# Performance work log

Measured on AMD Instinct MI355X. Metric: run time of the kernel, lower is better.

The kernel has to match this reference:

```python
import jax, jax.numpy as jnp
import numpy as np

B, C, H, W, T_PREV, HEADS, KSIZE = 16, 512, 28, 28, 15, 16, 5


def setup_inputs() -> dict:
    key = jax.random.key(0)
    ks = jax.random.split(key, 6)
    return {
        "x": jax.random.normal(ks[0], (B, C, H, W), jnp.float32),
        "prev_K": jax.random.normal(ks[1], (B, T_PREV, C), jnp.float32),
        "prev_V": jax.random.normal(ks[2], (B, T_PREV, C, H, W), jnp.float32) * 0.1,
        "wq": jax.random.normal(ks[3], (1, 1, KSIZE), jnp.float32) * 0.3,
        "wk": jax.random.normal(ks[4], (1, 1, KSIZE), jnp.float32) * 0.3,
        "wv": jax.random.normal(ks[5], (C, 1, 3, 3), jnp.float32) * 0.2,
    }


def _conv1d_same(y, ker):
    # y: [b,1,c], ker: [1,1,k]; SAME padding = (k-1)//2 on each side for odd k
    p = (ker.shape[-1] - 1) // 2
    return jax.lax.conv_general_dilated(
        y, ker, (1,), [(p, p)], dimension_numbers=("NCH", "OIH", "NCH"))


def _forward(x, prev_K, prev_V, wq, wk, wv):
    b, c, h, w = x.shape
    g = HEADS
    d = c // g
    norm = 1.0 / jnp.sqrt(jnp.asarray(d, x.dtype))
    # ECA-style channel attention: global avg pool -> conv1d over channels
    y = jnp.mean(x, axis=(2, 3))[:, None, :]            # [b,1,c]
    Q = _conv1d_same(y, wq)[:, 0, :]                    # [b,c]
    k = _conv1d_same(y, wk)                             # [b,1,c]
    # depthwise 3x3 conv for V
    v = jax.lax.conv_general_dilated(
        x, wv, (1, 1), [(1, 1), (1, 1)],
        dimension_numbers=("NCHW", "OIHW", "NCHW"), feature_group_count=c)
    # grow recurrent caches
    K = jnp.concatenate([prev_K, k], axis=1)            # [b,t,c]
    V = jnp.concatenate([prev_V, v[:, None]], axis=1)   # [b,t,c,h,w]
    t = K.shape[1]
    # grouped decode attention: single query step vs t cached steps
    Qg = Q.reshape(b, g, d)                             # [b,g,d]
    Kg = K.reshape(b, t, g, d)                          # [b,t,g,d]
    atten = jnp.einsum("bgd,btgd->bgt", Qg, Kg) * norm  # [b,g,t]
    atten = jax.nn.softmax(atten, axis=-1)
    Vg = V.reshape(b, t, g, d, h, w)                    # [b,t,g,d,h,w]
    out = jnp.einsum("bgt,btgdhw->bgdhw", atten, Vg).reshape(b, c, h, w)
    return out, K, V


def reference(x, prev_K, prev_V, wq, wk, wv):
    return _forward(x, prev_K, prev_V, wq, wk, wv)
```

## Files before the change

### kernel.cpp

```cpp
#include <hip/hip_runtime.h>
#include <hip/hip_bf16.h>

#define B_ 16
#define C_ 512
#define H_ 28
#define W_ 28
#define TPREV 15
#define TT 16
#define HEADS_ 16
#define DHEAD 32
#define HW 784
#define HW4 196
#define CH4 (C_ * HW4)
#define NORM 0.17677669529663687f

typedef float f32x4 __attribute__((ext_vector_type(4)));

__global__ __launch_bounds__(64) void pool_kernel(const float* __restrict__ x,
                                                  float* __restrict__ y) {
    const int bc = blockIdx.x;
    const f32x4* __restrict__ xr = (const f32x4*)(x + (size_t)bc * HW);
    const int lane = threadIdx.x;
    float s = 0.0f;
    for (int i = lane; i < HW4; i += 64) {
        f32x4 v = xr[i];
        s += v.x + v.y + v.z + v.w;
    }
    #pragma unroll
    for (int off = 32; off > 0; off >>= 1) s += __shfl_down(s, off);
    if (lane == 0) y[bc] = s * (1.0f / (float)HW);
}

__global__ __launch_bounds__(256) void attn_kernel(const float* __restrict__ y,
                                                   const float* __restrict__ prevK,
                                                   const float* __restrict__ wq,
                                                   const float* __restrict__ wk,
                                                   float* __restrict__ Kout,
                                                   float* __restrict__ att) {
    const int b = blockIdx.x;
    const int tid = threadIdx.x;
    __shared__ float y_s[C_];
    __shared__ float Q_s[C_];
    __shared__ float K_s[TT * 513];
    __shared__ float logit[HEADS_][17];

    y_s[tid]       = y[b * C_ + tid];
    y_s[tid + 256] = y[b * C_ + tid + 256];

    const float q0 = wq[0], q1 = wq[1], q2 = wq[2], q3 = wq[3], q4 = wq[4];
    const float k0 = wk[0], k1 = wk[1], k2 = wk[2], k3 = wk[3], k4 = wk[4];

    for (int i = tid; i < TPREV * C_; i += 256) {
        int t = i >> 9, c = i & (C_ - 1);
        K_s[t * 513 + c] = prevK[((size_t)b * TPREV + t) * C_ + c];
    }
    __syncthreads();

    for (int c = tid; c < C_; c += 256) {
        float a0 = (c >= 2)      ? y_s[c - 2] : 0.0f;
        float a1 = (c >= 1)      ? y_s[c - 1] : 0.0f;
        float a2 = y_s[c];
        float a3 = (c <= C_ - 2) ? y_s[c + 1] : 0.0f;
        float a4 = (c <= C_ - 3) ? y_s[c + 2] : 0.0f;
        Q_s[c]               = a0 * q0 + a1 * q1 + a2 * q2 + a3 * q3 + a4 * q4;
        K_s[TPREV * 513 + c] = a0 * k0 + a1 * k1 + a2 * k2 + a3 * k3 + a4 * k4;
    }
    __syncthreads();

    for (int i = tid; i < TT * C_; i += 256) {
        int t = i >> 9, c = i & (C_ - 1);
        Kout[((size_t)b * TT + t) * C_ + c] = K_s[t * 513 + c];
    }

    const int g = tid >> 4, t = tid & 15;
    float s = 0.0f;
    #pragma unroll
    for (int d = 0; d < DHEAD; ++d)
        s += Q_s[g * DHEAD + d] * K_s[t * 513 + g * DHEAD + d];
    s *= NORM;
    logit[g][t] = s;
    __syncthreads();

    float m = -1e30f;
    #pragma unroll
    for (int j = 0; j < TT; ++j) m = fmaxf(m, logit[g][j]);
    float sum = 0.0f;
    #pragma unroll
    for (int j = 0; j < TT; ++j) sum += __expf(logit[g][j] - m);
    att[((size_t)b * HEADS_ + g) * TT + t] = __expf(s - m) / sum;
}

__global__ __launch_bounds__(256) void fuse_kernel(const float* __restrict__ x,
                                                   const float* __restrict__ prevV,
                                                   const float* __restrict__ wv,
                                                   const float* __restrict__ att,
                                                   float* __restrict__ out,
                                                   float* __restrict__ Vout) {
    const int i = blockIdx.x * 256 + threadIdx.x;
    const int p4 = i % HW4;
    const int bc = i / HW4;
    const int c  = bc & (C_ - 1);
    const int b  = bc >> 9;
    const int g  = c >> 5;

    const float* __restrict__ xbc = x + (size_t)bc * HW;
    const int p  = p4 * 4;
    const int h  = p / W_;
    const int w0 = p % W_;
    float r[3][6];
    #pragma unroll
    for (int ry = 0; ry < 3; ++ry) {
        const int hh = h - 1 + ry;
        if (hh < 0 || hh >= H_) {
            #pragma unroll
            for (int j = 0; j < 6; ++j) r[ry][j] = 0.0f;
        } else {
            const float* row = xbc + hh * W_;
            f32x4 mid = *(const f32x4*)(row + w0);
            r[ry][1] = mid.x; r[ry][2] = mid.y; r[ry][3] = mid.z; r[ry][4] = mid.w;
            r[ry][0] = (w0 > 0)      ? row[w0 - 1] : 0.0f;
            r[ry][5] = (w0 + 4 < W_) ? row[w0 + 4] : 0.0f;
        }
    }
    float wv9[9];
    #pragma unroll
    for (int k = 0; k < 9; ++k) wv9[k] = wv[c * 9 + k];

    f32x4 v4;
    #pragma unroll
    for (int j = 0; j < 4; ++j) {
        float s = 0.0f;
        #pragma unroll
        for (int ky = 0; ky < 3; ++ky)
            #pragma unroll
            for (int kx = 0; kx < 3; ++kx)
                s = fmaf(r[ky][j + kx], wv9[ky * 3 + kx], s);
        v4[j] = s;
    }

    const float* __restrict__ arow = att + ((size_t)b * HEADS_ + g) * TT;

    f32x4* __restrict__ Vo = (f32x4*)Vout;
    const f32x4* __restrict__ Pv = (const f32x4*)prevV;
    const size_t pvq = ((size_t)b * TPREV * C_ + c) * HW4 + p4;
    const size_t voq = ((size_t)b * TT    * C_ + c) * HW4 + p4;

    f32x4 pv[TPREV];
    #pragma unroll
    for (int t = 0; t < TPREV; ++t)
        pv[t] = __builtin_nontemporal_load(&Pv[pvq + (size_t)t * CH4]);

    f32x4 acc;
    {
        const float a = arow[TPREV];
        __builtin_nontemporal_store(v4, &Vo[voq + (size_t)TPREV * CH4]);
        acc = v4 * a;
    }

    #pragma unroll
    for (int t = 0; t < TPREV; ++t) {
        __builtin_nontemporal_store(pv[t], &Vo[voq + (size_t)t * CH4]);
        const float a = arow[t];
        acc.x = fmaf(a, pv[t].x, acc.x);
        acc.y = fmaf(a, pv[t].y, acc.y);
        acc.z = fmaf(a, pv[t].z, acc.z);
        acc.w = fmaf(a, pv[t].w, acc.w);
    }
    __builtin_nontemporal_store(acc, &((f32x4*)out)[(size_t)bc * HW4 + p4]);
}

extern "C" void kernel_launch(void* const* d_in, const int* in_sizes, int n_in,
                              void* d_out, int out_size, void* d_ws, size_t ws_size,
                              hipStream_t stream) {
    const float* x     = (const float*)d_in[0];
    const float* prevK = (const float*)d_in[1];
    const float* prevV = (const float*)d_in[2];
    const float* wq    = (const float*)d_in[3];
    const float* wk    = (const float*)d_in[4];
    const float* wv    = (const float*)d_in[5];

    float* out  = (float*)d_out;
    float* Kout = out + (size_t)B_ * C_ * HW;
    float* Vout = Kout + (size_t)B_ * TT * C_;

    float* y_ws   = (float*)d_ws;
    float* att_ws = y_ws + B_ * C_;

    pool_kernel<<<B_ * C_, 64, 0, stream>>>(x, y_ws);
    attn_kernel<<<B_, 256, 0, stream>>>(y_ws, prevK, wq, wk, Kout, att_ws);

    const int totalq = B_ * C_ * HW4;
    fuse_kernel<<<totalq / 256, 256, 0, stream>>>(x, prevV, wv, att_ws, out, Vout);
}
```

Baseline: 161.0 us.

## Fold attention computation into fuse kernel and merge K copy into pool kernel

Removes the separate 16-block attention kernel. Each fuse block now recomputes Q, k and the softmax weights for the up to two channels it covers, using warp shuffles, and keeps them in shared memory. The prevK-to-Kout copy is appended as extra blocks of the pooling kernel. This cuts one launch and the serial low-occupancy attention stage, at the cost of redundant per-block attention work and a block-wide sync before the streaming loop. The prevV loads are hoisted ahead of that sync so their latency overlaps it.

```diff
diff --git a/kernel.cpp b/kernel.cpp
--- a/kernel.cpp
+++ b/kernel.cpp
@@ -16,92 +16,115 @@
 
 typedef float f32x4 __attribute__((ext_vector_type(4)));
 
-__global__ __launch_bounds__(64) void pool_kernel(const float* __restrict__ x,
-                                                  float* __restrict__ y) {
-    const int bc = blockIdx.x;
-    const f32x4* __restrict__ xr = (const f32x4*)(x + (size_t)bc * HW);
+#define POOL_BLOCKS (B_ * C_)
+#define KCOPY_QUADS (B_ * TPREV * C_ / 4)
+#define KCOPY_BLOCKS (KCOPY_QUADS / 64)
+
+__global__ __launch_bounds__(64) void pool_copy_kernel(const float* __restrict__ x,
+                                                       const float* __restrict__ prevK,
+                                                       float* __restrict__ y,
+                                                       float* __restrict__ Kout) {
     const int lane = threadIdx.x;
-    float s = 0.0f;
-    for (int i = lane; i < HW4; i += 64) {
-        f32x4 v = xr[i];
-        s += v.x + v.y + v.z + v.w;
-    }
-    #pragma unroll
-    for (int off = 32; off > 0; off >>= 1) s += __shfl_down(s, off);
-    if (lane == 0) y[bc] = s * (1.0f / (float)HW);
+    if (blockIdx.x < POOL_BLOCKS) {
+        const int bc = blockIdx.x;
+        const f32x4* __restrict__ xr = (const f32x4*)(x + (size_t)bc * HW);
+        float s = 0.0f;
+        for (int i = lane; i < HW4; i += 64) {
+            f32x4 v = xr[i];
+            s += v.x + v.y + v.z + v.w;
+        }
+        #pragma unroll
+        for (int off = 32; off > 0; off >>= 1) s += __shfl_down(s, off);
+        if (lane == 0) y[bc] = s * (1.0f / (float)HW);
+    } else {
+        const int j = (blockIdx.x - POOL_BLOCKS) * 64 + lane;
+        const f32x4* __restrict__ src = (const f32x4*)prevK;
+        f32x4* __restrict__ dst = (f32x4*)Kout;
+        const int b = j / (TPREV * C_ / 4);
+        dst[j + b * (C_ / 4)] = src[j];
+    }
 }
 
-__global__ __launch_bounds__(256) void attn_kernel(const float* __restrict__ y,
+__global__ __launch_bounds__(256) void fuse_kernel(const float* __restrict__ x,
+                                                   const float* __restrict__ prevV,
                                                    const float* __restrict__ prevK,
+                                                   const float* __restrict__ y,
                                                    const float* __restrict__ wq,
                                                    const float* __restrict__ wk,
+                                                   const float* __restrict__ wv,
+                                                   float* __restrict__ out,
                                                    float* __restrict__ Kout,
-                                                   float* __restrict__ att) {
-    const int b = blockIdx.x;
+                                                   float* __restrict__ Vout) {
     const int tid = threadIdx.x;
-    __shared__ float y_s[C_];
-    __shared__ float Q_s[C_];
-    __shared__ float K_s[TT * 513];
-    __shared__ float logit[HEADS_][17];
-
-    y_s[tid]       = y[b * C_ + tid];
-    y_s[tid + 256] = y[b * C_ + tid + 256];
-
-    const float q0 = wq[0], q1 = wq[1], q2 = wq[2], q3 = wq[3], q4 = wq[4];
-    const float k0 = wk[0], k1 = wk[1], k2 = wk[2], k3 = wk[3], k4 = wk[4];
-
-    for (int i = tid; i < TPREV * C_; i += 256) {
-        int t = i >> 9, c = i & (C_ - 1);
-        K_s[t * 513 + c] = prevK[((size_t)b * TPREV + t) * C_ + c];
+    const int blk0 = blockIdx.x * 256;
+    __shared__ float att_s[3][TT];
+
+    const int bc_lo = blk0 / HW4;
+    const int bc_hi = (blk0 + 255) / HW4;
+
+    if (tid < 96) {
+        const int half = tid >> 5;
+        const int d    = tid & 31;
+        const int bcx  = bc_lo + half;
+        if (bcx <= bc_hi) {
+            const int bb = bcx >> 9;
+            const int gg = (bcx & (C_ - 1)) >> 5;
+            const int cc = gg * DHEAD + d;
+
+            float Qc = 0.0f, kc = 0.0f;
+            #pragma unroll
+            for (int j = 0; j < 5; ++j) {
+                const int cj = cc - 2 + j;
+                const float yv = (cj >= 0 && cj < C_) ? y[bb * C_ + cj] : 0.0f;
+                Qc = fmaf(yv, wq[j], Qc);
+                kc = fmaf(yv, wk[j], kc);
+            }
+
+            float pl[TT];
+            #pragma unroll
+            for (int t = 0; t < TPREV; ++t)
+                pl[t] = Qc * prevK[((size_t)bb * TPREV + t) * C_ + cc];
+            pl[TPREV] = Qc * kc;
+
+            #pragma unroll
+            for (int m = 1; m <= 16; m <<= 1) {
+                #pragma unroll
+                for (int t = 0; t < TT; ++t)
+                    pl[t] += __shfl_xor(pl[t], m);
+            }
+
+            float mx = -1e30f;
+            #pragma unroll
+            for (int t = 0; t < TT; ++t) mx = fmaxf(mx, pl[t] * NORM);
+            float sum = 0.0f;
+            #pragma unroll
+            for (int t = 0; t < TT; ++t) sum += __expf(pl[t] * NORM - mx);
+            if (d < TT)
+                att_s[half][d] = __expf(pl[d] * NORM - mx) / sum;
+
+            const int qk = (bb * C_ + cc) * HW4;
+            if (qk >= blk0 && qk < blk0 + 256)
+                Kout[((size_t)bb * TT + TPREV) * C_ + cc] = kc;
+        }
     }
     __syncthreads();
 
-    for (int c = tid; c < C_; c += 256) {
-        float a0 = (c >= 2)      ? y_s[c - 2] : 0.0f;
-        float a1 = (c >= 1)      ? y_s[c - 1] : 0.0f;
-        float a2 = y_s[c];
-        float a3 = (c <= C_ - 2) ? y_s[c + 1] : 0.0f;
-        float a4 = (c <= C_ - 3) ? y_s[c + 2] : 0.0f;
-        Q_s[c]               = a0 * q0 + a1 * q1 + a2 * q2 + a3 * q3 + a4 * q4;
-        K_s[TPREV * 513 + c] = a0 * k0 + a1 * k1 + a2 * k2 + a3 * k3 + a4 * k4;
-    }
-    __syncthreads();
-
-    for (int i = tid; i < TT * C_; i += 256) {
-        int t = i >> 9, c = i & (C_ - 1);
-        Kout[((size_t)b * TT + t) * C_ + c] = K_s[t * 513 + c];
-    }
-
-    const int g = tid >> 4, t = tid & 15;
-    float s = 0.0f;
-    #pragma unroll
-    for (int d = 0; d < DHEAD; ++d)
-        s += Q_s[g * DHEAD + d] * K_s[t * 513 + g * DHEAD + d];
-    s *= NORM;
-    logit[g][t] = s;
-    __syncthreads();
-
-    float m = -1e30f;
-    #pragma unroll
-    for (int j = 0; j < TT; ++j) m = fmaxf(m, logit[g][j]);
-    float sum = 0.0f;
-    #pragma unroll
-    for (int j = 0; j < TT; ++j) sum += __expf(logit[g][j] - m);
-    att[((size_t)b * HEADS_ + g) * TT + t] = __expf(s - m) / sum;
-}
-
-__global__ __launch_bounds__(256) void fuse_kernel(const float* __restrict__ x,
-                                                   const float* __restrict__ prevV,
-                                                   const float* __restrict__ wv,
-                                                   const float* __restrict__ att,
-                                                   float* __restrict__ out,
-                                                   float* __restrict__ Vout) {
-    const int i = blockIdx.x * 256 + threadIdx.x;
+    const int i  = blk0 + tid;
     const int p4 = i % HW4;
     const int bc = i / HW4;
     const int c  = bc & (C_ - 1);
     const int b  = bc >> 9;
-    const int g  = c >> 5;
+    const int h_ = bc - bc_lo;
+
+    f32x4* __restrict__ Vo = (f32x4*)Vout;
+    const f32x4* __restrict__ Pv = (const f32x4*)prevV;
+    const size_t pvq = ((size_t)b * TPREV * C_ + c) * HW4 + p4;
+    const size_t voq = ((size_t)b * TT    * C_ + c) * HW4 + p4;
+
+    f32x4 pv[TPREV];
+    #pragma unroll
+    for (int t = 0; t < TPREV; ++t)
+        pv[t] = __builtin_nontemporal_load(&Pv[pvq + (size_t)t * CH4]);
 
     const float* __restrict__ xbc = x + (size_t)bc * HW;
     const int p  = p4 * 4;
@@ -138,21 +161,9 @@
         v4[j] = s;
     }
 
-    const float* __restrict__ arow = att + ((size_t)b * HEADS_ + g) * TT;
-
-    f32x4* __restrict__ Vo = (f32x4*)Vout;
-    const f32x4* __restrict__ Pv = (const f32x4*)prevV;
-    const size_t pvq = ((size_t)b * TPREV * C_ + c) * HW4 + p4;
-    const size_t voq = ((size_t)b * TT    * C_ + c) * HW4 + p4;
-
-    f32x4 pv[TPREV];
-    #pragma unroll
-    for (int t = 0; t < TPREV; ++t)
-        pv[t] = __builtin_nontemporal_load(&Pv[pvq + (size_t)t * CH4]);
-
     f32x4 acc;
     {
-        const float a = arow[TPREV];
+        const float a = att_s[h_][TPREV];
         __builtin_nontemporal_store(v4, &Vo[voq + (size_t)TPREV * CH4]);
         acc = v4 * a;
     }
@@ -160,7 +171,7 @@
     #pragma unroll
     for (int t = 0; t < TPREV; ++t) {
         __builtin_nontemporal_store(pv[t], &Vo[voq + (size_t)t * CH4]);
-        const float a = arow[t];
+        const float a = att_s[h_][t];
         acc.x = fmaf(a, pv[t].x, acc.x);
         acc.y = fmaf(a, pv[t].y, acc.y);
         acc.z = fmaf(a, pv[t].z, acc.z);
@@ -183,12 +194,11 @@
     float* Kout = out + (size_t)B_ * C_ * HW;
     float* Vout = Kout + (size_t)B_ * TT * C_;
 
-    float* y_ws   = (float*)d_ws;
-    float* att_ws = y_ws + B_ * C_;
-
-    pool_kernel<<<B_ * C_, 64, 0, stream>>>(x, y_ws);
-    attn_kernel<<<B_, 256, 0, stream>>>(y_ws, prevK, wq, wk, Kout, att_ws);
+    float* y_ws = (float*)d_ws;
+
+    pool_copy_kernel<<<POOL_BLOCKS + KCOPY_BLOCKS, 64, 0, stream>>>(x, prevK, y_ws, Kout);
 
     const int totalq = B_ * C_ * HW4;
-    fuse_kernel<<<totalq / 256, 256, 0, stream>>>(x, prevV, wv, att_ws, out, Vout);
+    fuse_kernel<<<totalq / 256, 256, 0, stream>>>(x, prevV, prevK, y_ws, wq, wk, wv,
+                                                  out, Kout, Vout);
 }
```

Result: no change. 159.9 us, median of 2 (-0.7%).
